# Kernel tuning notes

Measured on AMD Instinct MI355X. Metric: run time of the kernel, lower is better.

## Reference

```python
import jax, jax.numpy as jnp
import numpy as np


def setup_inputs() -> dict:
    key = jax.random.key(0)
    k1, k2, k3, k4 = jax.random.split(key, 4)
    B, N, Fin, Fout, K = 8, 256, 64, 64, 3
    H = jax.random.normal(k1, (B, N, N, Fin), dtype=jnp.float32)
    # static Chebyshev polynomial stacks T_0..T_{K-1} for origin / dest Laplacians
    cheb_L1 = jax.random.normal(k2, (K, N, N), dtype=jnp.float32) * 0.1
    cheb_L2 = jax.random.normal(k3, (K, N, N), dtype=jnp.float32) * 0.1
    # xavier_uniform over last two dims (fan_in=Fin, fan_out=Fout)
    limit = float(np.sqrt(6.0 / (Fin + Fout)))
    weights = jax.random.uniform(k4, (K, K, Fin, Fout), dtype=jnp.float32,
                                 minval=-limit, maxval=limit)
    bias = jnp.zeros((Fout,), dtype=jnp.float32)
    return {"H": H, "cheb_L1": cheb_L1, "cheb_L2": cheb_L2,
            "weights": weights, "bias": bias}


def reference(H, cheb_L1, cheb_L2, weights, bias):
    # H' = relu( sum_{i,j} T_i(L1) @_1 H @_2 T_j(L2) @_3 W_ij + b )
    # Step 1: left graph shift for all i at once: (K,B,N,N,F)
    H_x1 = jnp.einsum('kuv,bvwf->kbuwf', cheb_L1, H)
    # Step 2+3 fused: right shift by T_j, project by W_ij, accumulate over i,j
    out = jnp.einsum('kbuwf,lwz,klfo->buzo', H_x1, cheb_L2, weights)
    return jax.nn.relu(out + bias)
```

## Files before the change

kernel.cpp:

```cpp
#include <hip/hip_runtime.h>

typedef __attribute__((ext_vector_type(8))) short s16x8;
typedef __attribute__((ext_vector_type(4))) float f32x4;

#define MFMA16 __builtin_amdgcn_mfma_f32_16x16x32_bf16
#define WAITVM(N) asm volatile("s_waitcnt vmcnt(" #N ")" ::: "memory")
#define SBAR() asm volatile("s_barrier" ::: "memory")
#define WAITLGKM0() asm volatile("s_waitcnt lgkmcnt(0)" ::: "memory")
#define SCHEDB() __builtin_amdgcn_sched_barrier(0)

__device__ __forceinline__ short f2bf(float x) {
  union { float f; unsigned u; } c; c.f = x;
  unsigned r = (c.u + 0x7fffu + ((c.u >> 16) & 1u)) >> 16;
  return (short)r;
}

__device__ __forceinline__ void gld16(const void* g, void* l) {
  __builtin_amdgcn_global_load_lds(
      (const __attribute__((address_space(1))) unsigned*)g,
      (__attribute__((address_space(3))) unsigned*)l, 16, 0, 0);
}


__global__ __launch_bounds__(256) void k_cvt_l1(const float* __restrict__ L1,
                                                short* __restrict__ L1b) {
  int i = blockIdx.x * 256 + threadIdx.x;
  L1b[i] = f2bf(L1[i]);
}

__global__ __launch_bounds__(256) void k_build_l2cat(const float* __restrict__ L2,
                                                     short* __restrict__ L2cat) {
  __shared__ float t[32][33];
  const int l = blockIdx.z, w0 = blockIdx.x * 32, z0 = blockIdx.y * 32;
  const int tx = threadIdx.x, ty = threadIdx.y;
  const float* src = L2 + (size_t)l * 65536;
  for (int i = ty; i < 32; i += 8) t[i][tx] = src[(size_t)(w0 + i) * 256 + z0 + tx];
  __syncthreads();
  for (int i = ty; i < 32; i += 8)
    L2cat[(size_t)(z0 + i) * 768 + l * 256 + w0 + tx] = f2bf(t[tx][i]);
}

__global__ __launch_bounds__(256) void k_build_wt(const float* __restrict__ W,
                                                  short* __restrict__ WT) {
  for (int idx = threadIdx.x + blockIdx.x * 256; idx < 192 * 192; idx += 256 * gridDim.x) {
    int lo = idx / 192, kf = idx % 192;
    int l = lo >> 6, o = lo & 63, k = kf / 64, f = kf & 63;
    WT[idx] = f2bf(W[(((size_t)(k * 3 + l) * 64 + f) << 6) + o]);
  }
}

__global__ __launch_bounds__(256) void k_cvt_ht(const float* __restrict__ H,
                                                short* __restrict__ HbT, int b0) {
  __shared__ float t[32][33];
  const int bc = blockIdx.z;
  const int wf0 = blockIdx.x * 32, v0 = blockIdx.y * 32;
  const int tx = threadIdx.x, ty = threadIdx.y;
  const float* src = H + ((size_t)(b0 + bc) * 256 + v0) * 16384;
  for (int i = ty; i < 32; i += 8) t[i][tx] = src[(size_t)i * 16384 + wf0 + tx];
  __syncthreads();
  short* dst = HbT + ((size_t)bc * 16384 + wf0) * 256;
  for (int i = ty; i < 32; i += 8) dst[(size_t)i * 256 + v0 + tx] = f2bf(t[tx][i]);
}

__global__ __launch_bounds__(256, 4) void k_s1(const short* __restrict__ L1b,
                                               const short* __restrict__ HbT,
                                               short* __restrict__ A2) {
  __shared__ __align__(16) short At[2][128 * 32];
  __shared__ __align__(16) short Bt[2][128 * 32];
  const int t = threadIdx.x, lane = t & 63, wid = t >> 6;
  const int n0 = blockIdx.x * 128;
  const int kk = blockIdx.y >> 1;
  const int u0 = (blockIdx.y & 1) * 128;
  const int bc = blockIdx.z;
  const short* Ag = L1b + (size_t)kk * 65536;
  const short* Bg = HbT + (size_t)bc * 16384 * 256;
  const int wm = wid >> 1, wn = wid & 1;
  const int srow = lane >> 2;
  const int selem = ((lane & 3) ^ ((lane >> 3) & 3)) * 8;
  const int koff = ((lane >> 4) ^ ((lane >> 1) & 3)) * 8;
  const int ar = lane & 15;
#pragma unroll
  for (int j = 0; j < 2; ++j) {
    const int rb = wid * 32 + j * 16;
    gld16(Ag + (size_t)(u0 + rb + srow) * 256 + selem, At[0] + rb * 32);
    gld16(Bg + (size_t)(n0 + rb + srow) * 256 + selem, Bt[0] + rb * 32);
  }
  __syncthreads();
  f32x4 acc[4][4] = {};
#pragma unroll
  for (int kt8 = 0; kt8 < 8; ++kt8) {
    const int cur = kt8 & 1;
    s16x8 a[4], b[4];
#pragma unroll
    for (int i = 0; i < 4; ++i)
      a[i] = *(const s16x8*)&At[cur][(wm * 64 + i * 16 + ar) * 32 + koff];
#pragma unroll
    for (int j = 0; j < 4; ++j)
      b[j] = *(const s16x8*)&Bt[cur][(wn * 64 + j * 16 + ar) * 32 + koff];
    if (kt8 < 7) {
#pragma unroll
      for (int j = 0; j < 2; ++j) {
        const int rb = wid * 32 + j * 16;
        gld16(Ag + (size_t)(u0 + rb + srow) * 256 + (kt8 + 1) * 32 + selem, At[cur ^ 1] + rb * 32);
        gld16(Bg + (size_t)(n0 + rb + srow) * 256 + (kt8 + 1) * 32 + selem, Bt[cur ^ 1] + rb * 32);
      }
    }
#pragma unroll
    for (int i = 0; i < 4; ++i)
#pragma unroll
      for (int j = 0; j < 4; ++j) acc[i][j] = MFMA16(a[i], b[j], acc[i][j], 0, 0, 0);
    __syncthreads();
  }
  const int cr = lane >> 4, cc = lane & 15;
#pragma unroll
  for (int i = 0; i < 4; ++i)
#pragma unroll
    for (int j = 0; j < 4; ++j) {
      const int ncol = n0 + wn * 64 + j * 16 + cc;
      const int w = ncol >> 6, f = ncol & 63;
#pragma unroll
      for (int r = 0; r < 4; ++r) {
        const int u = u0 + wm * 64 + i * 16 + cr * 4 + r;
        A2[(((size_t)bc * 256 + u) * 256 + w) * 192 + kk * 64 + f] = f2bf(acc[i][j][r]);
      }
    }
}

__global__ __launch_bounds__(512, 2) void k_s23(const short* __restrict__ A2,
                                                const short* __restrict__ WTg,
                                                const short* __restrict__ L2cat,
                                                const float* __restrict__ bias,
                                                float* __restrict__ out, int b0) {
  __shared__ __align__(16) short P[64 * 768];
  __shared__ __align__(16) short AtS[8][3][32 * 32];
  short* Ws = P;
  const int t = threadIdx.x, lane = t & 63, wid = t >> 6;
  const int bul = blockIdx.x;
  const int ar = lane & 15, cc = ar, cr = lane >> 4, sl = lane & 7, ks = lane >> 4;
  const int srow = lane >> 2;
  const int selem = ((lane & 3) ^ ((lane >> 3) & 3)) * 8;
  const int koff = ((lane >> 4) ^ ((lane >> 1) & 3)) * 8;
  const short* A2g = A2 + (size_t)bul * 49152;

#define P1S(tt, bi)                                                                        \
  do {                                                                                     \
    gld16(A2g + (size_t)(wid * 32 + srow) * 192 + (tt) * 32 + selem, &AtS[wid][bi][0]);    \
    gld16(A2g + (size_t)(wid * 32 + 16 + srow) * 192 + (tt) * 32 + selem,                  \
          &AtS[wid][bi][512]);                                                             \
  } while (0)
#define P2S(tt, bi)                                                                        \
  do {                                                                                     \
    gld16(L2cat + (size_t)(wid * 32 + srow) * 768 + (tt) * 32 + selem, &AtS[wid][bi][0]);  \
    gld16(L2cat + (size_t)(wid * 32 + 16 + srow) * 768 + (tt) * 32 + selem,                \
          &AtS[wid][bi][512]);                                                             \
  } while (0)

  P1S(0, 0);
  P1S(1, 1);
  P1S(2, 2);
  for (int s = wid; s < 72; s += 8) {
    const int t6 = s / 12, g = (s % 12) * 16;
    gld16(WTg + (size_t)(g + srow) * 192 + t6 * 32 + selem, Ws + ((size_t)t6 * 192 + g) * 32);
  }
  __syncthreads();

  f32x4 acc[12][2] = {};
#pragma unroll
  for (int kt6 = 0; kt6 < 6; ++kt6) {
    if (kt6 == 3) { WAITVM(4); } else if (kt6 == 4) { WAITVM(2); } else if (kt6 == 5) { WAITVM(0); }
    const short* stc = &AtS[wid][kt6 % 3][0];
    s16x8 a0 = *(const s16x8*)&stc[(0 + ar) * 32 + koff];
    s16x8 a1 = *(const s16x8*)&stc[(16 + ar) * 32 + koff];
#pragma unroll
    for (int j2 = 0; j2 < 12; ++j2) {
      s16x8 b = *(const s16x8*)&Ws[((size_t)kt6 * 192 + j2 * 16 + ar) * 32 + koff];
      acc[j2][0] = MFMA16(a0, b, acc[j2][0], 0, 0, 0);
      acc[j2][1] = MFMA16(a1, b, acc[j2][1], 0, 0, 0);
    }
    SCHEDB();
    if (kt6 == 0) { P1S(3, 0); } else if (kt6 == 1) { P1S(4, 1); } else if (kt6 == 2) { P1S(5, 2); }
  }
  WAITLGKM0();
  SBAR();

  P2S(0, 0);
  P2S(1, 1);
  P2S(2, 2);

#pragma unroll
  for (int j2 = 0; j2 < 12; ++j2)
#pragma unroll
    for (int i = 0; i < 2; ++i)
#pragma unroll
      for (int rp = 0; rp < 2; ++rp) {
        const int r = rp * 2;
        const int w = wid * 32 + i * 16 + cr * 4 + r;
        const int lo = j2 * 16 + cc;
        const int l = lo >> 6, o = lo & 63;
        const int lw = l * 256 + w;
        const int addr = o * 768 + ((lw >> 3) ^ (o & 7)) * 8 + (lw & 7);
        unsigned lo16 = (unsigned short)f2bf(acc[j2][i][r]);
        unsigned hi16 = (unsigned short)f2bf(acc[j2][i][r + 1]);
        *(unsigned*)&P[addr] = lo16 | (hi16 << 16);
      }
  WAITLGKM0();
  SBAR();

  f32x4 acc2[2][4] = {};
#pragma unroll
  for (int t2 = 0; t2 < 24; ++t2) {
    if (t2 < 22) { WAITVM(4); } else if (t2 == 22) { WAITVM(2); } else { WAITVM(0); }
    const short* stc = &AtS[wid][t2 % 3][0];
    s16x8 a0 = *(const s16x8*)&stc[(0 + ar) * 32 + koff];
    s16x8 a1 = *(const s16x8*)&stc[(16 + ar) * 32 + koff];
    const int S = t2 * 4 + ks;
#pragma unroll
    for (int j = 0; j < 4; ++j) {
      s16x8 b = *(const s16x8*)&P[(j * 16 + ar) * 768 + (S ^ sl) * 8];
      acc2[0][j] = MFMA16(a0, b, acc2[0][j], 0, 0, 0);
      acc2[1][j] = MFMA16(a1, b, acc2[1][j], 0, 0, 0);
    }
    SCHEDB();
    if (t2 < 21) {
      if (t2 % 3 == 0) { P2S(t2 + 3, 0); } else if (t2 % 3 == 1) { P2S(t2 + 3, 1); } else { P2S(t2 + 3, 2); }
    }
  }
#undef P1S
#undef P2S

  float* og = out + ((size_t)b0 * 256 + bul) * 16384;
#pragma unroll
  for (int i = 0; i < 2; ++i)
#pragma unroll
    for (int j = 0; j < 4; ++j) {
      const float bv = bias[j * 16 + cc];
#pragma unroll
      for (int r = 0; r < 4; ++r) {
        const int z = wid * 32 + i * 16 + cr * 4 + r;
        og[(size_t)z * 64 + j * 16 + cc] = fmaxf(acc2[i][j][r] + bv, 0.f);
      }
    }
}

extern "C" void kernel_launch(void* const* d_in, const int* in_sizes, int n_in,
                              void* d_out, int out_size, void* d_ws, size_t ws_size,
                              hipStream_t stream) {
  const float* H    = (const float*)d_in[0];
  const float* L1   = (const float*)d_in[1];
  const float* L2   = (const float*)d_in[2];
  const float* W    = (const float*)d_in[3];
  const float* bias = (const float*)d_in[4];
  float* out = (float*)d_out;

  char* ws = (char*)d_ws;
  short* L1b   = (short*)ws;
  short* L2cat = (short*)(ws + (384 << 10));
  short* WT    = (short*)(ws + (768 << 10));
  char* data = ws + (4ull << 20);

  const size_t perb = 32ull << 20;
  size_t avail = (ws_size > (4ull << 20)) ? ws_size - (4ull << 20) : 0;
  int nb = 1;
  if (avail >= 8 * perb) nb = 8;
  else if (avail >= 4 * perb) nb = 4;
  else if (avail >= 2 * perb) nb = 2;

  short* HbT = (short*)data;
  short* A2  = (short*)(data + (size_t)nb * (8ull << 20));

  k_cvt_l1<<<768, 256, 0, stream>>>(L1, L1b);
  k_build_l2cat<<<dim3(8, 8, 3), dim3(32, 8), 0, stream>>>(L2, L2cat);
  k_build_wt<<<36, 256, 0, stream>>>(W, WT);

  for (int b0 = 0; b0 < 8; b0 += nb) {
    k_cvt_ht<<<dim3(512, 8, nb), dim3(32, 8), 0, stream>>>(H, HbT, b0);
    k_s1<<<dim3(128, 6, nb), 256, 0, stream>>>(L1b, HbT, A2);
    k_s23<<<nb * 256, 512, 0, stream>>>(A2, WT, L2cat, bias, out, b0);
  }
}
```

Baseline: 323.6 us.

## Load MFMA operands directly from global memory instead of LDS staging

Removes the LDS double/triple-buffered async global-to-LDS staging in both GEMM kernels (k_s1 and the A2/L2cat operand streams in k_s23) and has each wave read its MFMA fragments straight from global memory into registers. The goal is to drop the barriers, waitcnt choreography and LDS traffic. The cost is uncoalesced, strided 16-byte global reads with no explicit prefetch, and operands shared between waves are re-read through cache. k_s1's launch bounds also drop from 4 to 3 waves per SIMD.

After: 439.2 us. 1.36x slower.

```diff
diff --git a/kernel.cpp b/kernel.cpp
--- a/kernel.cpp
+++ b/kernel.cpp
@@ -4,10 +4,8 @@
 typedef __attribute__((ext_vector_type(4))) float f32x4;
 
 #define MFMA16 __builtin_amdgcn_mfma_f32_16x16x32_bf16
-#define WAITVM(N) asm volatile("s_waitcnt vmcnt(" #N ")" ::: "memory")
 #define SBAR() asm volatile("s_barrier" ::: "memory")
 #define WAITLGKM0() asm volatile("s_waitcnt lgkmcnt(0)" ::: "memory")
-#define SCHEDB() __builtin_amdgcn_sched_barrier(0)
 
 __device__ __forceinline__ short f2bf(float x) {
   union { float f; unsigned u; } c; c.f = x;
@@ -62,11 +60,9 @@
   for (int i = ty; i < 32; i += 8) dst[(size_t)i * 256 + v0 + tx] = f2bf(t[tx][i]);
 }
 
-__global__ __launch_bounds__(256, 4) void k_s1(const short* __restrict__ L1b,
+__global__ __launch_bounds__(256, 3) void k_s1(const short* __restrict__ L1b,
                                                const short* __restrict__ HbT,
                                                short* __restrict__ A2) {
-  __shared__ __align__(16) short At[2][128 * 32];
-  __shared__ __align__(16) short Bt[2][128 * 32];
   const int t = threadIdx.x, lane = t & 63, wid = t >> 6;
   const int n0 = blockIdx.x * 128;
   const int kk = blockIdx.y >> 1;
@@ -75,41 +71,21 @@
   const short* Ag = L1b + (size_t)kk * 65536;
   const short* Bg = HbT + (size_t)bc * 16384 * 256;
   const int wm = wid >> 1, wn = wid & 1;
-  const int srow = lane >> 2;
-  const int selem = ((lane & 3) ^ ((lane >> 3) & 3)) * 8;
-  const int koff = ((lane >> 4) ^ ((lane >> 1) & 3)) * 8;
-  const int ar = lane & 15;
-#pragma unroll
-  for (int j = 0; j < 2; ++j) {
-    const int rb = wid * 32 + j * 16;
-    gld16(Ag + (size_t)(u0 + rb + srow) * 256 + selem, At[0] + rb * 32);
-    gld16(Bg + (size_t)(n0 + rb + srow) * 256 + selem, Bt[0] + rb * 32);
-  }
-  __syncthreads();
+  const int ar = lane & 15, ks8 = (lane >> 4) * 8;
   f32x4 acc[4][4] = {};
 #pragma unroll
-  for (int kt8 = 0; kt8 < 8; ++kt8) {
-    const int cur = kt8 & 1;
+  for (int kt = 0; kt < 8; ++kt) {
     s16x8 a[4], b[4];
 #pragma unroll
     for (int i = 0; i < 4; ++i)
-      a[i] = *(const s16x8*)&At[cur][(wm * 64 + i * 16 + ar) * 32 + koff];
+      a[i] = *(const s16x8*)&Ag[(size_t)(u0 + wm * 64 + i * 16 + ar) * 256 + kt * 32 + ks8];
 #pragma unroll
     for (int j = 0; j < 4; ++j)
-      b[j] = *(const s16x8*)&Bt[cur][(wn * 64 + j * 16 + ar) * 32 + koff];
-    if (kt8 < 7) {
-#pragma unroll
-      for (int j = 0; j < 2; ++j) {
-        const int rb = wid * 32 + j * 16;
-        gld16(Ag + (size_t)(u0 + rb + srow) * 256 + (kt8 + 1) * 32 + selem, At[cur ^ 1] + rb * 32);
-        gld16(Bg + (size_t)(n0 + rb + srow) * 256 + (kt8 + 1) * 32 + selem, Bt[cur ^ 1] + rb * 32);
-      }
-    }
+      b[j] = *(const s16x8*)&Bg[(size_t)(n0 + wn * 64 + j * 16 + ar) * 256 + kt * 32 + ks8];
 #pragma unroll
     for (int i = 0; i < 4; ++i)
 #pragma unroll
       for (int j = 0; j < 4; ++j) acc[i][j] = MFMA16(a[i], b[j], acc[i][j], 0, 0, 0);
-    __syncthreads();
   }
   const int cr = lane >> 4, cc = lane & 15;
 #pragma unroll
@@ -132,32 +108,16 @@
                                                 const float* __restrict__ bias,
                                                 float* __restrict__ out, int b0) {
   __shared__ __align__(16) short P[64 * 768];
-  __shared__ __align__(16) short AtS[8][3][32 * 32];
   short* Ws = P;
   const int t = threadIdx.x, lane = t & 63, wid = t >> 6;
   const int bul = blockIdx.x;
   const int ar = lane & 15, cc = ar, cr = lane >> 4, sl = lane & 7, ks = lane >> 4;
+  const int ks8 = ks * 8;
   const int srow = lane >> 2;
   const int selem = ((lane & 3) ^ ((lane >> 3) & 3)) * 8;
   const int koff = ((lane >> 4) ^ ((lane >> 1) & 3)) * 8;
   const short* A2g = A2 + (size_t)bul * 49152;
 
-#define P1S(tt, bi)                                                                        \
-  do {                                                                                     \
-    gld16(A2g + (size_t)(wid * 32 + srow) * 192 + (tt) * 32 + selem, &AtS[wid][bi][0]);    \
-    gld16(A2g + (size_t)(wid * 32 + 16 + srow) * 192 + (tt) * 32 + selem,                  \
-          &AtS[wid][bi][512]);                                                             \
-  } while (0)
-#define P2S(tt, bi)                                                                        \
-  do {                                                                                     \
-    gld16(L2cat + (size_t)(wid * 32 + srow) * 768 + (tt) * 32 + selem, &AtS[wid][bi][0]);  \
-    gld16(L2cat + (size_t)(wid * 32 + 16 + srow) * 768 + (tt) * 32 + selem,                \
-          &AtS[wid][bi][512]);                                                             \
-  } while (0)
-
-  P1S(0, 0);
-  P1S(1, 1);
-  P1S(2, 2);
   for (int s = wid; s < 72; s += 8) {
     const int t6 = s / 12, g = (s % 12) * 16;
     gld16(WTg + (size_t)(g + srow) * 192 + t6 * 32 + selem, Ws + ((size_t)t6 * 192 + g) * 32);
@@ -167,25 +127,17 @@
   f32x4 acc[12][2] = {};
 #pragma unroll
   for (int kt6 = 0; kt6 < 6; ++kt6) {
-    if (kt6 == 3) { WAITVM(4); } else if (kt6 == 4) { WAITVM(2); } else if (kt6 == 5) { WAITVM(0); }
-    const short* stc = &AtS[wid][kt6 % 3][0];
-    s16x8 a0 = *(const s16x8*)&stc[(0 + ar) * 32 + koff];
-    s16x8 a1 = *(const s16x8*)&stc[(16 + ar) * 32 + koff];
+    s16x8 a0 = *(const s16x8*)&A2g[(size_t)(wid * 32 + ar) * 192 + kt6 * 32 + ks8];
+    s16x8 a1 = *(const s16x8*)&A2g[(size_t)(wid * 32 + 16 + ar) * 192 + kt6 * 32 + ks8];
 #pragma unroll
     for (int j2 = 0; j2 < 12; ++j2) {
       s16x8 b = *(const s16x8*)&Ws[((size_t)kt6 * 192 + j2 * 16 + ar) * 32 + koff];
       acc[j2][0] = MFMA16(a0, b, acc[j2][0], 0, 0, 0);
       acc[j2][1] = MFMA16(a1, b, acc[j2][1], 0, 0, 0);
     }
-    SCHEDB();
-    if (kt6 == 0) { P1S(3, 0); } else if (kt6 == 1) { P1S(4, 1); } else if (kt6 == 2) { P1S(5, 2); }
   }
   WAITLGKM0();
   SBAR();
-
-  P2S(0, 0);
-  P2S(1, 1);
-  P2S(2, 2);
 
 #pragma unroll
   for (int j2 = 0; j2 < 12; ++j2)
@@ -209,10 +161,8 @@
   f32x4 acc2[2][4] = {};
 #pragma unroll
   for (int t2 = 0; t2 < 24; ++t2) {
-    if (t2 < 22) { WAITVM(4); } else if (t2 == 22) { WAITVM(2); } else { WAITVM(0); }
-    const short* stc = &AtS[wid][t2 % 3][0];
-    s16x8 a0 = *(const s16x8*)&stc[(0 + ar) * 32 + koff];
-    s16x8 a1 = *(const s16x8*)&stc[(16 + ar) * 32 + koff];
+    s16x8 a0 = *(const s16x8*)&L2cat[(size_t)(wid * 32 + ar) * 768 + t2 * 32 + ks8];
+    s16x8 a1 = *(const s16x8*)&L2cat[(size_t)(wid * 32 + 16 + ar) * 768 + t2 * 32 + ks8];
     const int S = t2 * 4 + ks;
 #pragma unroll
     for (int j = 0; j < 4; ++j) {
@@ -220,13 +170,7 @@
       acc2[0][j] = MFMA16(a0, b, acc2[0][j], 0, 0, 0);
       acc2[1][j] = MFMA16(a1, b, acc2[1][j], 0, 0, 0);
     }
-    SCHEDB();
-    if (t2 < 21) {
-      if (t2 % 3 == 0) { P2S(t2 + 3, 0); } else if (t2 % 3 == 1) { P2S(t2 + 3, 1); } else { P2S(t2 + 3, 2); }
-    }
-  }
-#undef P1S
-#undef P2S
+  }
 
   float* og = out + ((size_t)b0 * 256 + bul) * 16384;
 #pragma unroll
```

## Split stage-2/3 kernel over l to cut LDS and registers for higher occupancy

Applied to the files above, without the earlier changes.

The fused projection+right-shift kernel now processes the three Chebyshev l terms sequentially. For each l it computes only a 64-wide slice of the W projection into a 64x256 LDS tile, then accumulates that slice's contribution against L2cat. This shrinks the P buffer threefold and the first accumulator from 12x2 to 4x2 tiles, and launch bounds are raised to 4 blocks per CU. In exchange the A2 tiles are reloaded three times, and there are extra barriers and pipeline restarts per l.

Result: no change. 322.1 us (-0.5%).

```diff
diff --git a/kernel.cpp b/kernel.cpp
--- a/kernel.cpp
+++ b/kernel.cpp
@@ -44,7 +44,7 @@
                                                   short* __restrict__ WT) {
   for (int idx = threadIdx.x + blockIdx.x * 256; idx < 192 * 192; idx += 256 * gridDim.x) {
     int lo = idx / 192, kf = idx % 192;
-    int l = lo >> 6, o = lo & 63, k = kf / 64, f = kf & 63;
+    int l = lo / 64, o = lo & 63, k = kf / 64, f = kf & 63;
     WT[idx] = f2bf(W[(((size_t)(k * 3 + l) * 64 + f) << 6) + o]);
   }
 }
@@ -126,12 +126,12 @@
     }
 }
 
-__global__ __launch_bounds__(512, 2) void k_s23(const short* __restrict__ A2,
+__global__ __launch_bounds__(512, 4) void k_s23(const short* __restrict__ A2,
                                                 const short* __restrict__ WTg,
                                                 const short* __restrict__ L2cat,
                                                 const float* __restrict__ bias,
                                                 float* __restrict__ out, int b0) {
-  __shared__ __align__(16) short P[64 * 768];
+  __shared__ __align__(16) short P[64 * 256];
   __shared__ __align__(16) short AtS[8][3][32 * 32];
   short* Ws = P;
   const int t = threadIdx.x, lane = t & 63, wid = t >> 6;
@@ -155,74 +155,83 @@
           &AtS[wid][bi][512]);                                                             \
   } while (0)
 
-  P1S(0, 0);
-  P1S(1, 1);
-  P1S(2, 2);
-  for (int s = wid; s < 72; s += 8) {
-    const int t6 = s / 12, g = (s % 12) * 16;
-    gld16(WTg + (size_t)(g + srow) * 192 + t6 * 32 + selem, Ws + ((size_t)t6 * 192 + g) * 32);
-  }
-  __syncthreads();
-
-  f32x4 acc[12][2] = {};
-#pragma unroll
-  for (int kt6 = 0; kt6 < 6; ++kt6) {
-    if (kt6 == 3) { WAITVM(4); } else if (kt6 == 4) { WAITVM(2); } else if (kt6 == 5) { WAITVM(0); }
-    const short* stc = &AtS[wid][kt6 % 3][0];
-    s16x8 a0 = *(const s16x8*)&stc[(0 + ar) * 32 + koff];
-    s16x8 a1 = *(const s16x8*)&stc[(16 + ar) * 32 + koff];
-#pragma unroll
-    for (int j2 = 0; j2 < 12; ++j2) {
-      s16x8 b = *(const s16x8*)&Ws[((size_t)kt6 * 192 + j2 * 16 + ar) * 32 + koff];
-      acc[j2][0] = MFMA16(a0, b, acc[j2][0], 0, 0, 0);
-      acc[j2][1] = MFMA16(a1, b, acc[j2][1], 0, 0, 0);
-    }
-    SCHEDB();
-    if (kt6 == 0) { P1S(3, 0); } else if (kt6 == 1) { P1S(4, 1); } else if (kt6 == 2) { P1S(5, 2); }
-  }
-  WAITLGKM0();
-  SBAR();
-
-  P2S(0, 0);
-  P2S(1, 1);
-  P2S(2, 2);
-
-#pragma unroll
-  for (int j2 = 0; j2 < 12; ++j2)
-#pragma unroll
-    for (int i = 0; i < 2; ++i)
-#pragma unroll
-      for (int rp = 0; rp < 2; ++rp) {
-        const int r = rp * 2;
-        const int w = wid * 32 + i * 16 + cr * 4 + r;
-        const int lo = j2 * 16 + cc;
-        const int l = lo >> 6, o = lo & 63;
-        const int lw = l * 256 + w;
-        const int addr = o * 768 + ((lw >> 3) ^ (o & 7)) * 8 + (lw & 7);
-        unsigned lo16 = (unsigned short)f2bf(acc[j2][i][r]);
-        unsigned hi16 = (unsigned short)f2bf(acc[j2][i][r + 1]);
-        *(unsigned*)&P[addr] = lo16 | (hi16 << 16);
-      }
-  WAITLGKM0();
-  SBAR();
-
   f32x4 acc2[2][4] = {};
 #pragma unroll
-  for (int t2 = 0; t2 < 24; ++t2) {
-    if (t2 < 22) { WAITVM(4); } else if (t2 == 22) { WAITVM(2); } else { WAITVM(0); }
-    const short* stc = &AtS[wid][t2 % 3][0];
-    s16x8 a0 = *(const s16x8*)&stc[(0 + ar) * 32 + koff];
-    s16x8 a1 = *(const s16x8*)&stc[(16 + ar) * 32 + koff];
-    const int S = t2 * 4 + ks;
-#pragma unroll
-    for (int j = 0; j < 4; ++j) {
-      s16x8 b = *(const s16x8*)&P[(j * 16 + ar) * 768 + (S ^ sl) * 8];
-      acc2[0][j] = MFMA16(a0, b, acc2[0][j], 0, 0, 0);
-      acc2[1][j] = MFMA16(a1, b, acc2[1][j], 0, 0, 0);
-    }
-    SCHEDB();
-    if (t2 < 21) {
-      if (t2 % 3 == 0) { P2S(t2 + 3, 0); } else if (t2 % 3 == 1) { P2S(t2 + 3, 1); } else { P2S(t2 + 3, 2); }
+  for (int l = 0; l < 3; ++l) {
+    const short* WTl = WTg + (size_t)l * 64 * 192;
+    for (int s = wid; s < 24; s += 8) {
+      const int t6 = s / 4, g = (s & 3) * 16;
+      gld16(WTl + (size_t)(g + srow) * 192 + t6 * 32 + selem, Ws + ((size_t)t6 * 64 + g) * 32);
+    }
+    P1S(0, 0);
+    P1S(1, 1);
+    P1S(2, 2);
+    WAITVM(6);
+    SBAR();
+
+    f32x4 acc[4][2] = {};
+#pragma unroll
+    for (int kt6 = 0; kt6 < 6; ++kt6) {
+      if (kt6 < 4) { WAITVM(4); } else if (kt6 == 4) { WAITVM(2); } else { WAITVM(0); }
+      const short* stc = &AtS[wid][kt6 % 3][0];
+      s16x8 a0 = *(const s16x8*)&stc[(0 + ar) * 32 + koff];
+      s16x8 a1 = *(const s16x8*)&stc[(16 + ar) * 32 + koff];
+#pragma unroll
+      for (int j2 = 0; j2 < 4; ++j2) {
+        s16x8 b = *(const s16x8*)&Ws[((size_t)kt6 * 64 + j2 * 16 + ar) * 32 + koff];
+        acc[j2][0] = MFMA16(a0, b, acc[j2][0], 0, 0, 0);
+        acc[j2][1] = MFMA16(a1, b, acc[j2][1], 0, 0, 0);
+      }
+      SCHEDB();
+      if (kt6 == 0) { P1S(3, 0); } else if (kt6 == 1) { P1S(4, 1); } else if (kt6 == 2) { P1S(5, 2); }
+    }
+    WAITLGKM0();
+    SBAR();
+
+    P2S(l * 8 + 0, 0);
+    P2S(l * 8 + 1, 1);
+    P2S(l * 8 + 2, 2);
+
+#pragma unroll
+    for (int j2 = 0; j2 < 4; ++j2)
+#pragma unroll
+      for (int i = 0; i < 2; ++i)
+#pragma unroll
+        for (int rp = 0; rp < 2; ++rp) {
+          const int r = rp * 2;
+          const int w = wid * 32 + i * 16 + cr * 4 + r;
+          const int o = j2 * 16 + cc;
+          const int addr = o * 256 + (((w >> 3) ^ (o & 7)) << 3) + (w & 7);
+          unsigned lo16 = (unsigned short)f2bf(acc[j2][i][r]);
+          unsigned hi16 = (unsigned short)f2bf(acc[j2][i][r + 1]);
+          *(unsigned*)&P[addr] = lo16 | (hi16 << 16);
+        }
+    WAITLGKM0();
+    SBAR();
+
+#pragma unroll
+    for (int t2 = 0; t2 < 8; ++t2) {
+      if (t2 < 6) { WAITVM(4); } else if (t2 == 6) { WAITVM(2); } else { WAITVM(0); }
+      const short* stc = &AtS[wid][t2 % 3][0];
+      s16x8 a0 = *(const s16x8*)&stc[(0 + ar) * 32 + koff];
+      s16x8 a1 = *(const s16x8*)&stc[(16 + ar) * 32 + koff];
+      const int S = t2 * 4 + ks;
+#pragma unroll
+      for (int j = 0; j < 4; ++j) {
+        s16x8 b = *(const s16x8*)&P[(j * 16 + ar) * 256 + ((S ^ sl) << 3)];
+        acc2[0][j] = MFMA16(a0, b, acc2[0][j], 0, 0, 0);
+        acc2[1][j] = MFMA16(a1, b, acc2[1][j], 0, 0, 0);
+      }
+      SCHEDB();
+      if (t2 < 5) {
+        if (t2 % 3 == 0) { P2S(l * 8 + t2 + 3, 0); }
+        else if (t2 % 3 == 1) { P2S(l * 8 + t2 + 3, 1); }
+        else { P2S(l * 8 + t2 + 3, 2); }
+      }
+    }
+    if (l < 2) {
+      WAITLGKM0();
+      SBAR();
     }
   }
 #undef P1S
```
